# Performance work log

Measured on AMD Instinct MI355X. Metric: run time of the kernel, lower is better.

Reference implementation:

```python
import jax, jax.numpy as jnp
import numpy as np

EPS = 1e-4
SLOPE = 0.01
NFFT = 512
HOP = 256
CH_IN = 8
CH_H = 64
FREQ = NFFT // 2 + 1
LEN = 48000
BATCH = 2


def hann(n):
    return (0.5 - 0.5 * jnp.cos(2.0 * np.pi * jnp.arange(n) / n)).astype(jnp.float32)


def stft(x):
    # x: (B, C, L) -> (B, 2, C, F, T)  (torch.stft: center=True, reflect pad, hann window)
    pad = NFFT // 2
    xp = jnp.pad(x, ((0, 0), (0, 0), (pad, pad)), mode='reflect')
    T = 1 + x.shape[-1] // HOP
    idx = jnp.arange(T)[:, None] * HOP + jnp.arange(NFFT)[None, :]
    frames = xp[..., idx] * hann(NFFT)            # (B, C, T, NFFT)
    sp = jnp.fft.rfft(frames, axis=-1)            # (B, C, T, F)
    sp = jnp.swapaxes(sp, -1, -2)                 # (B, C, F, T)
    return jnp.stack([sp.real, sp.imag], axis=1).astype(jnp.float32)


def istft(re, im, length):
    # re, im: (B, C, F, T) -> (B, C, length) via windowed overlap-add
    sp = jnp.swapaxes(re + 1j * im, -1, -2)       # (B, C, T, F)
    win = hann(NFFT)
    frames = jnp.fft.irfft(sp, n=NFFT, axis=-1) * win
    pad = NFFT // 2
    total = length + 2 * pad
    T = frames.shape[-2]
    idx = jnp.arange(T)[:, None] * HOP + jnp.arange(NFFT)[None, :]
    out = jnp.zeros(frames.shape[:-2] + (total,), frames.dtype).at[..., idx].add(frames)
    wsum = jnp.zeros((total,), frames.dtype).at[idx].add(jnp.broadcast_to(win ** 2, (T, NFFT)))
    return (out / jnp.maximum(wsum, 1e-11))[..., pad:pad + length]


def conv2d(x, w, b, padT=0):
    y = jax.lax.conv_general_dilated(x, w, (1, 1), ((0, 0), (padT, padT)),
                                     dimension_numbers=('NCHW', 'OIHW', 'NCHW'))
    return y + b[None, :, None, None]


def cconv(x, w, b, padT=0):
    # complex conv on x: (B,2,C,F,T); w: (2,O,C,kf,kt) = [W_real, W_imag]; b: (2,O)
    r = conv2d(x[:, 0], w[0], b[0], padT) - conv2d(x[:, 1], w[1], b[1], padT)
    i = conv2d(x[:, 1], w[0], b[0], padT) + conv2d(x[:, 0], w[1], b[1], padT)
    return jnp.stack([r, i], axis=1)


def modExp(x, m=5.0):
    em = float(np.exp(m))
    return jnp.where(x > m, (x - m) * em + em, jnp.exp(jnp.minimum(x, m)))


def cExp(t):
    e = modExp(t[:, 0]) - 1.0
    return jnp.stack([e * jnp.cos(t[:, 1] - 1.0), e * jnp.sin(t[:, 1] - 1.0)], axis=1)


def snap(x):
    x = jnp.where((x >= 0) & (x < EPS), EPS, x)
    return jnp.where((x < 0) & (x > -EPS), -EPS, x)


def cLog(t):
    re = snap(t[:, 0])
    im = snap(t[:, 1])
    real = jnp.log(jnp.sqrt(im ** 2 + re ** 2 + EPS ** 2) + 1.0)
    imag = jnp.arctan(im / re)
    return jnp.stack([real, imag], axis=1)


def cMul(a, b):
    r = a[:, 0] * b[:, 0] - a[:, 1] * b[:, 1]
    i = a[:, 0] * b[:, 1] + a[:, 1] * b[:, 0]
    return jnp.stack([r, i], axis=1)


def trelu(t, tr, b):
    nr = t[:, 0] * tr[0, 0] + t[:, 1] * tr[0, 1] + b[0]
    ni = t[:, 0] * tr[1, 0] + t[:, 1] * tr[1, 1] + b[1]
    return jnp.stack([jax.nn.leaky_relu(nr, SLOPE), jax.nn.leaky_relu(ni, SLOPE)], axis=1)


def tgate(t, tr, b):
    gr = jax.nn.sigmoid(t[:, 0] * tr[0, 0] + t[:, 1] * tr[0, 1] + b[0])
    gi = jax.nn.sigmoid(t[:, 0] * tr[1, 0] + t[:, 1] * tr[1, 1] + b[1])
    return gr * gi + (1.0 - gr) * (1.0 - gi)


def perm(t):
    return jnp.transpose(t, (0, 1, 3, 2, 4))


def lrelu(x):
    return jax.nn.leaky_relu(x, SLOPE)


def forward(mix, fs_w, fs_b, fr_w, fr_b, c1r_w, c1r_b, c1i_w, c1i_b, c1_w, c1_b,
            c2r_w, c2r_b, c2i_w, c2i_b, c2_w, c2_b, a1_t, a1_b, a2_t, a2_b,
            c3r_w, c3r_b, c3i_w, c3i_b, c3_w, c3_b, c4r_w, c4r_b, c4i_w, c4i_b,
            c4_w, c4_b, a3_t, a3_b, a4_t, a4_b, f1_w, f1_b, f2_w, f2_b,
            cw_w, cw_b, fg_t, fg_b):
    ts = perm(cconv(perm(stft(mix)), fs_w, fs_b))      # (B,2,C,F,T)
    # ---- branch 1 ----
    tl = cLog(ts)
    tl = jnp.stack([conv2d(tl[:, 0], c1r_w, c1r_b), conv2d(tl[:, 1], c1r_w, c1r_b)], 1)
    tl = jnp.stack([conv2d(lrelu(tl[:, 0]), c1i_w, c1i_b), conv2d(tl[:, 1], c1i_w, c1i_b)], 1)
    tl = trelu(cExp(tl), a1_t, a1_b)
    t = cconv(tl, c1_w, c1_b)
    tl = cLog(t)
    tl = jnp.stack([conv2d(tl[:, 0], c2r_w, c2r_b, 7), conv2d(tl[:, 1], c2r_w, c2r_b, 7)], 1)[..., :-7]
    tl = jnp.stack([conv2d(lrelu(tl[:, 0]), c2i_w, c2i_b, 7), conv2d(tl[:, 1], c2i_w, c2i_b, 7)], 1)[..., :-7]
    tl = cExp(tl)
    tl1 = tl
    tc = cconv(ts, c2_w, c2_b, 7)[..., :-7]
    t = trelu(cMul(tl, tc), a2_t, a2_b)
    t = cconv(t, f1_w, f1_b)
    td1 = jnp.sum(ts - t, axis=2, keepdims=True) / ts.shape[2]
    # ---- branch 2 ----
    tl = cLog(ts)
    tl = jnp.stack([conv2d(tl[:, 0], c3r_w, c3r_b), conv2d(tl[:, 1], c3r_w, c3r_b)], 1)
    tl = jnp.stack([conv2d(lrelu(tl[:, 0]), c3i_w, c3i_b), conv2d(tl[:, 1], c3i_w, c3i_b)], 1)
    tl = trelu(cExp(tl), a3_t, a3_b)
    t = cconv(tl, c3_w, c3_b)
    tl = cLog(t)
    tl = jnp.stack([conv2d(tl[:, 0], c4r_w, c4r_b, 7), conv2d(tl[:, 1], c4r_w, c4r_b, 7)], 1)[..., :-7]
    tl = jnp.stack([conv2d(lrelu(tl[:, 0]), c4i_w, c4i_b, 7), conv2d(tl[:, 1], c4i_w, c4i_b, 7)], 1)[..., :-7]
    tl = cExp(tl)
    tc = cconv(ts, c4_w, c4_b, 7)[..., :-7]
    t = trelu(cMul(tl, tc), a4_t, a4_b)
    td2 = cconv(t, f2_w, f2_b)                         # (B,2,1,F,T)
    # ---- fuse ----
    f = cconv(jnp.concatenate([tl1, tl], axis=2), cw_w, cw_b)
    f = tgate(f, fg_t, fg_b)[:, None]                  # (B,1,1,F,T)
    td = td1 * f + td2 * (1.0 - f)
    t = perm(cconv(perm(td), fr_w, fr_b))
    return istft(t[:, 0], t[:, 1], LEN)                # (B,1,LEN)


def setup_inputs() -> dict:
    ks = iter(jax.random.split(jax.random.key(0), 64))
    def rn(shape, s=0.05):
        return s * jax.random.normal(next(ks), shape, jnp.float32)
    F, C, H = FREQ, CH_IN, CH_H
    inp = {
        'mix': jax.random.normal(next(ks), (BATCH, C, LEN), jnp.float32),
        'fs_w': rn((2, F, F, 1, 1)), 'fs_b': rn((2, F), 0.01),
        'fr_w': rn((2, F, F, 1, 1)), 'fr_b': rn((2, F), 0.01),
        'c1r_w': rn((H, C, 1, 1)), 'c1r_b': rn((H,), 0.01),
        'c1i_w': rn((H, H, 1, 1)), 'c1i_b': rn((H,), 0.01),
        'c1_w': rn((2, H, H, 1, 1)), 'c1_b': rn((2, H), 0.01),
        'c2r_w': rn((H, H, 1, 8)), 'c2r_b': rn((H,), 0.01),
        'c2i_w': rn((H, H, 1, 8)), 'c2i_b': rn((H,), 0.01),
        'c2_w': rn((2, H, C, 1, 8)), 'c2_b': rn((2, H), 0.01),
        'a1_t': rn((2, 2, H, F, 1), 0.5), 'a1_b': rn((2, H, F, 1), 0.5),
        'a2_t': rn((2, 2, H, F, 1), 0.5), 'a2_b': rn((2, H, F, 1), 0.5),
        'c3r_w': rn((H, C, 1, 1)), 'c3r_b': rn((H,), 0.01),
        'c3i_w': rn((H, H, 1, 1)), 'c3i_b': rn((H,), 0.01),
        'c3_w': rn((2, H, H, 1, 1)), 'c3_b': rn((2, H), 0.01),
        'c4r_w': rn((H, H, 1, 8)), 'c4r_b': rn((H,), 0.01),
        'c4i_w': rn((H, H, 1, 8)), 'c4i_b': rn((H,), 0.01),
        'c4_w': rn((2, H, C, 1, 8)), 'c4_b': rn((2, H), 0.01),
        'a3_t': rn((2, 2, H, F, 1), 0.5), 'a3_b': rn((2, H, F, 1), 0.5),
        'a4_t': rn((2, 2, H, F, 1), 0.5), 'a4_b': rn((2, H, F, 1), 0.5),
        'f1_w': rn((2, C, H, 1, 1)), 'f1_b': rn((2, C), 0.01),
        'f2_w': rn((2, 1, H, 1, 1)), 'f2_b': rn((2, 1), 0.01),
        'cw_w': rn((2, 1, 2 * H, 1, 1)), 'cw_b': rn((2, 1), 0.01),
        'fg_t': rn((2, 2, 1, F, 1), 0.5), 'fg_b': rn((2, 1, F, 1), 0.5),
    }
    return inp


def reference(mix, fs_w, fs_b, fr_w, fr_b, c1r_w, c1r_b, c1i_w, c1i_b, c1_w, c1_b,
              c2r_w, c2r_b, c2i_w, c2i_b, c2_w, c2_b, a1_t, a1_b, a2_t, a2_b,
              c3r_w, c3r_b, c3i_w, c3i_b, c3_w, c3_b, c4r_w, c4r_b, c4i_w, c4i_b,
              c4_w, c4_b, a3_t, a3_b, a4_t, a4_b, f1_w, f1_b, f2_w, f2_b,
              cw_w, cw_b, fg_t, fg_b):
    return forward(mix, fs_w, fs_b, fr_w, fr_b, c1r_w, c1r_b, c1i_w, c1i_b, c1_w, c1_b,
                   c2r_w, c2r_b, c2i_w, c2i_b, c2_w, c2_b, a1_t, a1_b, a2_t, a2_b,
                   c3r_w, c3r_b, c3i_w, c3i_b, c3_w, c3_b, c4r_w, c4r_b, c4i_w, c4i_b,
                   c4_w, c4_b, a3_t, a3_b, a4_t, a4_b, f1_w, f1_b, f2_w, f2_b,
                   cw_w, cw_b, fg_t, fg_b)
```

## Files before the change

### kernel.cpp

```cpp
#include <hip/hip_runtime.h>
#include <math.h>

#define DEV __device__ __forceinline__

constexpr int B_   = 2;
constexpr int C_IN = 8;
constexpr int H_   = 64;
constexpr int F_   = 257;
constexpr int T_   = 188;
constexpr int TW   = 96;
constexpr int NFFT = 512;
constexpr int HOP  = 256;
constexpr int LEN  = 48000;
constexpr int PADL = 256;
constexpr int FT   = F_ * T_;
constexpr float EPSV  = 1e-4f;
constexpr float SLOPEV = 0.01f;
constexpr float PI2 = 6.283185307179586f;

typedef __attribute__((ext_vector_type(8))) short short8;
typedef __attribute__((ext_vector_type(4))) float float4v;

DEV float lrelu_f(float x) { return x > 0.f ? x : SLOPEV * x; }
DEV float snap_f(float x) {
  if (x >= 0.f && x < EPSV) return EPSV;
  if (x < 0.f && x > -EPSV) return -EPSV;
  return x;
}
DEV float modexp_f(float x) {
  const float em = 148.4131591025766f;
  return x > 5.f ? (x - 5.f) * em + em : expf(x);
}
DEV void cexp_f(float tr, float ti, float& er, float& ei) {
  float e = modexp_f(tr) - 1.f;
  float s, c;
  sincosf(ti - 1.f, &s, &c);
  er = e * c; ei = e * s;
}
DEV float sigmoid_f(float x) { return 1.f / (1.f + expf(-x)); }

DEV short f2bf(float x) {
  unsigned u = __float_as_uint(x);
  unsigned r = (u + 0x7fffu + ((u >> 16) & 1u)) >> 16;
  return (short)r;
}
DEV float bf2f(short h) {
  return __uint_as_float(((unsigned)(unsigned short)h) << 16);
}

__global__ __launch_bounds__(320) void k_stft(const float* __restrict__ mix,
                                              float* __restrict__ out) {
  __shared__ float xw[NFFT], xu[256], xv[256];
  int blk = blockIdx.x;
  int t = blk % T_;
  int bc = blk / T_;
  int c = bc % C_IN;
  int b = bc / C_IN;
  int tid = threadIdx.x;
  for (int n = tid; n < NFFT; n += 320) {
    int g = t * HOP + n - PADL;
    if (g < 0) g = -g;
    if (g >= LEN) g = 2 * LEN - 2 - g;
    float win = 0.5f - 0.5f * cosf((PI2 / NFFT) * n);
    xw[n] = mix[(b * C_IN + c) * LEN + g] * win;
  }
  __syncthreads();
  for (int n = tid + 1; n < 256; n += 320) {
    xu[n] = xw[n] + xw[NFFT - n];
    xv[n] = xw[n] - xw[NFFT - n];
  }
  __syncthreads();
  int f = tid;
  if (f < F_) {
    float sd, cd;
    sincosf((PI2 / NFFT) * f, &sd, &cd);
    float cs = cd, sn = sd, re = 0.f, im = 0.f;
    for (int n = 1; n < 256; ++n) {
      re += xu[n] * cs;
      im -= xv[n] * sn;
      float t2 = cs * cd - sn * sd;
      sn = sn * cd + cs * sd;
      cs = t2;
    }
    re += xw[0] + xw[256] * (1.f - 2.f * (f & 1));
    out[((b * 2 + 0) * C_IN + c) * FT + f * T_ + t] = re;
    out[((b * 2 + 1) * C_IN + c) * FT + f * T_ + t] = im;
  }
}

template<int CH>
__global__ void k_fmix(const float* __restrict__ X, const float* __restrict__ W,
                       const float* __restrict__ bias, float* __restrict__ Y) {
  int fo = blockIdx.x;
  int bc = blockIdx.y; int c = bc % CH; int b = bc / CH;
  int t = threadIdx.x;
  if (t >= T_) return;
  const float* wr = W + fo * F_;
  const float* wi = W + F_ * F_ + fo * F_;
  const float* xr = X + ((b * 2 + 0) * CH + c) * FT + t;
  const float* xi = X + ((b * 2 + 1) * CH + c) * FT + t;
  float ar = 0.f, ai = 0.f;
  for (int fi = 0; fi < F_; ++fi) {
    float wrv = wr[fi], wiv = wi[fi];
    float xrv = xr[fi * T_], xiv = xi[fi * T_];
    ar += wrv * xrv - wiv * xiv;
    ai += wrv * xiv + wiv * xrv;
  }
  float br = bias[fo], bi = bias[F_ + fo];
  Y[((b * 2 + 0) * CH + c) * FT + fo * T_ + t] = ar + br - bi;
  Y[((b * 2 + 1) * CH + c) * FT + fo * T_ + t] = ai + br + bi;
}

template<int CIN, int K>
DEV void repack_real_body(const float* __restrict__ W, short* __restrict__ wpk, int i) {
  constexpr int CC = (CIN >= 32) ? (CIN / 32) : 1;
  constexpr int NSTEP = (CIN * K + 31) / 32;
  int total = 2 * NSTEP * 4 * 64 * 8;
  if (i >= total) return;
  int j = i & 7;
  int lane = (i >> 3) & 63;
  int mt = (i >> 9) & 3;
  int s = (i >> 11) % NSTEP;
  int split = i / (NSTEP * 2048);
  int q = lane >> 4;
  int m = mt * 16 + (lane & 15);
  int tap = s / CC;
  int c = (s % CC) * 32 + q * 8 + j;
  float w = 0.f;
  if (c < CIN && tap < K) w = W[(m * CIN + c) * K + tap];
  short hi = f2bf(w);
  wpk[i] = split ? f2bf(w - bf2f(hi)) : hi;
}

template<int CIN2, int COUT2, int K>
DEV void repack_cplx_body(const float* __restrict__ W, short* __restrict__ wpk, int i) {
  constexpr int CIN = CIN2 / 2, COUT = COUT2 / 2;
  constexpr int NSTEP = CIN2 * K / 32;
  constexpr int MT = (COUT2 + 15) / 16;
  int total = 2 * NSTEP * MT * 64 * 8;
  if (i >= total) return;
  int j = i & 7;
  int lane = (i >> 3) & 63;
  int idx = i >> 9;
  int mt = idx % MT; idx /= MT;
  int s = idx % NSTEP;
  int split = idx / NSTEP;
  int q = lane >> 4;
  int m = mt * 16 + (lane & 15);
  int tap, pi, ci;
  if constexpr (CIN2 == 128) {
    tap = 0;
    int cs = s * 32 + q * 8 + j;
    int half = cs / 64, r = cs % 64;
    ci = half * 32 + r / 2;
    pi = r & 1;
  } else {
    tap = s * 2 + (q >> 1);
    int cs = (q & 1) * 8 + j;
    pi = cs / CIN;
    ci = cs % CIN;
  }
  float w = 0.f;
  if (m < COUT2) {
    int po = m / COUT, ho = m % COUT;
    float wr = W[((0 * COUT + ho) * CIN + ci) * K + tap];
    float wi = W[((1 * COUT + ho) * CIN + ci) * K + tap];
    w = (po == pi) ? wr : (po == 0 ? -wi : wi);
  }
  short hi = f2bf(w);
  wpk[i] = split ? f2bf(w - bf2f(hi)) : hi;
}

__global__ __launch_bounds__(256) void k_repack_all(
    const float* c1r_w, const float* c1i_w, const float* c2r_w, const float* c2i_w,
    const float* c3r_w, const float* c3i_w, const float* c4r_w, const float* c4i_w,
    const float* c1_w, const float* c2_w, const float* c3_w, const float* c4_w,
    const float* f1_w, const float* f2_w,
    short* o0, short* o1, short* o2, short* o3, short* o4, short* o5, short* o6,
    short* o7, short* o8, short* o9, short* o10, short* o11, short* o12, short* o13) {
  int i = blockIdx.x * 256 + threadIdx.x;
  switch (blockIdx.y) {
    case 0:  repack_real_body<C_IN, 1>(c1r_w, o0, i); break;
    case 1:  repack_real_body<H_,   1>(c1i_w, o1, i); break;
    case 2:  repack_real_body<H_,   8>(c2r_w, o2, i); break;
    case 3:  repack_real_body<H_,   8>(c2i_w, o3, i); break;
    case 4:  repack_real_body<C_IN, 1>(c3r_w, o4, i); break;
    case 5:  repack_real_body<H_,   1>(c3i_w, o5, i); break;
    case 6:  repack_real_body<H_,   8>(c4r_w, o6, i); break;
    case 7:  repack_real_body<H_,   8>(c4i_w, o7, i); break;
    case 8:  repack_cplx_body<128, 128, 1>(c1_w, o8, i); break;
    case 9:  repack_cplx_body<16,  128, 8>(c2_w, o9, i); break;
    case 10: repack_cplx_body<128, 128, 1>(c3_w, o10, i); break;
    case 11: repack_cplx_body<16,  128, 8>(c4_w, o11, i); break;
    case 12: repack_cplx_body<128, 16,  1>(f1_w, o12, i); break;
    case 13: repack_cplx_body<128, 2,   1>(f2_w, o13, i); break;
  }
}

template<int CIN, int K, int PRO>
__global__ __launch_bounds__(256) void k_conv_mfma(
    const float* __restrict__ X, const short* __restrict__ wpk,
    const float* __restrict__ bias, float* __restrict__ Y) {
  constexpr int CC = (CIN >= 32) ? (CIN / 32) : 1;
  constexpr int NSTEP = (CIN * K + 31) / 32;
  constexpr int PITCH = 72;
  constexpr int ROWS = TW + (K - 1);
  __shared__ short xs_hi[ROWS * PITCH];
  __shared__ short xs_lo[ROWS * PITCH];
  int f = blockIdx.x;
  int bp = blockIdx.y; int p = bp & 1; int b = bp >> 1;
  int t0 = blockIdx.z * TW;
  int tid = threadIdx.x;

  for (int i = tid; i < ROWS * PITCH; i += 256) { xs_hi[i] = 0; xs_lo[i] = 0; }
  __syncthreads();

  const float* Xr_ = X + (size_t)((b * 2 + 0) * CIN) * FT + f * T_;
  const float* Xi_ = X + (size_t)((b * 2 + 1) * CIN) * FT + f * T_;
  const float* Xp  = X + (size_t)((b * 2 + p) * CIN) * FT + f * T_;
  for (int i = tid; i < CIN * ROWS; i += 256) {
    int c = i / ROWS, rr = i % ROWS;
    int t = t0 + rr - (K - 1);
    if (t < 0 || t >= T_) continue;
    float v;
    if (PRO == 2) {
      float re = snap_f(Xr_[c * FT + t]);
      float im = snap_f(Xi_[c * FT + t]);
      v = (p == 0) ? logf(sqrtf(im * im + re * re + EPSV * EPSV) + 1.f)
                   : atanf(im / re);
    } else {
      v = Xp[c * FT + t];
      if (PRO == 1 && p == 0) v = lrelu_f(v);
    }
    short hi = f2bf(v);
    short lo = f2bf(v - bf2f(hi));
    xs_hi[rr * PITCH + c] = hi;
    xs_lo[rr * PITCH + c] = lo;
  }
  __syncthreads();

  int lane = tid & 63;
  int wv = __builtin_amdgcn_readfirstlane(tid >> 6);
  int mh = wv >> 1;
  int tc = wv & 1;
  int q = lane >> 4;
  int n = lane & 15;
  int wbase = tc * 48;

  float4v acc[2][3];
  #pragma unroll
  for (int mt = 0; mt < 2; ++mt)
    #pragma unroll
    for (int nt = 0; nt < 3; ++nt) acc[mt][nt] = (float4v)(0.f);

  const short8* wp = (const short8*)wpk;
  for (int s = 0; s < NSTEP; ++s) {
    int tap = s / CC;
    int c0 = (s % CC) * 32;
    short8 Bh[3], Bl[3];
    #pragma unroll
    for (int nt = 0; nt < 3; ++nt) {
      int off = (wbase + nt * 16 + n + tap) * PITCH + c0 + q * 8;
      Bh[nt] = *(const short8*)&xs_hi[off];
      Bl[nt] = *(const short8*)&xs_lo[off];
    }
    #pragma unroll
    for (int mt = 0; mt < 2; ++mt) {
      int mtg = mh * 2 + mt;
      short8 Ah = wp[((0 * NSTEP + s) * 4 + mtg) * 64 + lane];
      short8 Al = wp[((1 * NSTEP + s) * 4 + mtg) * 64 + lane];
      #pragma unroll
      for (int nt = 0; nt < 3; ++nt) {
        acc[mt][nt] = __builtin_amdgcn_mfma_f32_16x16x32_bf16(Ah, Bh[nt], acc[mt][nt], 0, 0, 0);
        acc[mt][nt] = __builtin_amdgcn_mfma_f32_16x16x32_bf16(Ah, Bl[nt], acc[mt][nt], 0, 0, 0);
        acc[mt][nt] = __builtin_amdgcn_mfma_f32_16x16x32_bf16(Al, Bh[nt], acc[mt][nt], 0, 0, 0);
      }
    }
  }

  float* Yp = Y + (size_t)((b * 2 + p) * H_) * FT + f * T_;
  #pragma unroll
  for (int nt = 0; nt < 3; ++nt) {
    int t = t0 + wbase + nt * 16 + n;
    if (t >= T_) continue;
    #pragma unroll
    for (int mt = 0; mt < 2; ++mt) {
      #pragma unroll
      for (int r = 0; r < 4; ++r) {
        int h = (mh * 2 + mt) * 16 + q * 4 + r;
        Yp[h * FT + t] = acc[mt][nt][r] + bias[h];
      }
    }
  }
}

template<int COUT2, int PRO>
__global__ __launch_bounds__(256) void k_cconv128(
    const float* __restrict__ X0, const float* __restrict__ X1,
    const short* __restrict__ wpk,
    const float* __restrict__ at, const float* __restrict__ ab,
    const float* __restrict__ bias, float* __restrict__ Y) {
  constexpr int MT = (COUT2 + 15) / 16;
  constexpr int MTW = (MT > 4) ? 4 : MT;
  constexpr int COUT = COUT2 / 2;
  constexpr int NSTEP = 4;
  constexpr int PITCH = 72;
  __shared__ short xs_hi[TW * PITCH];
  __shared__ short xs_lo[TW * PITCH];
  __shared__ float coef[6][64];
  int f = blockIdx.x;
  int b = blockIdx.y;
  int t0 = blockIdx.z * TW;
  int tid = threadIdx.x;
  int lane = tid & 63;
  int wv = __builtin_amdgcn_readfirstlane(tid >> 6);
  int mh = wv >> 1;
  int tc = wv & 1;
  int q = lane >> 4;
  int n = lane & 15;
  int wbase = tc * 48;

  if (tid < 64) {
    int h = tid;
    coef[0][h] = at[(0 * H_ + h) * F_ + f];
    coef[1][h] = at[(1 * H_ + h) * F_ + f];
    coef[2][h] = at[(2 * H_ + h) * F_ + f];
    coef[3][h] = at[(3 * H_ + h) * F_ + f];
    coef[4][h] = ab[h * F_ + f];
    coef[5][h] = ab[(H_ + h) * F_ + f];
  }
  for (int i = tid; i < TW * PITCH; i += 256) { xs_hi[i] = 0; xs_lo[i] = 0; }

  const float* b0r = X0 + (size_t)((b * 2 + 0) * H_) * FT + f * T_;
  const float* b0i = X0 + (size_t)((b * 2 + 1) * H_) * FT + f * T_;
  const float* b1r = X1 + (size_t)((b * 2 + 0) * H_) * FT + f * T_;
  const float* b1i = X1 + (size_t)((b * 2 + 1) * H_) * FT + f * T_;

  float4v acc[MTW][3];
  #pragma unroll
  for (int mt = 0; mt < MTW; ++mt)
    #pragma unroll
    for (int nt = 0; nt < 3; ++nt) acc[mt][nt] = (float4v)(0.f);

  const short8* wp = (const short8*)wpk;
  for (int half = 0; half < 2; ++half) {
    __syncthreads();
    for (int i = tid; i < 32 * TW; i += 256) {
      int hh = i / TW, tl = i % TW;
      int t = t0 + tl;
      if (t >= T_) continue;
      int h = half * 32 + hh;
      float xr = b0r[h * FT + t], xi = b0i[h * FT + t];
      float vr, vi;
      if (PRO == 1) {
        float er, ei;
        cexp_f(xr, xi, er, ei);
        vr = lrelu_f(er * coef[0][h] + ei * coef[1][h] + coef[4][h]);
        vi = lrelu_f(er * coef[2][h] + ei * coef[3][h] + coef[5][h]);
      } else {
        float yr = b1r[h * FT + t], yi = b1i[h * FT + t];
        float mr = xr * yr - xi * yi;
        float mi = xr * yi + xi * yr;
        vr = lrelu_f(mr * coef[0][h] + mi * coef[1][h] + coef[4][h]);
        vi = lrelu_f(mr * coef[2][h] + mi * coef[3][h] + coef[5][h]);
      }
      int cs0 = hh * 2, cs1 = hh * 2 + 1;
      short hr = f2bf(vr), hi2 = f2bf(vi);
      xs_hi[tl * PITCH + cs0] = hr;
      xs_lo[tl * PITCH + cs0] = f2bf(vr - bf2f(hr));
      xs_hi[tl * PITCH + cs1] = hi2;
      xs_lo[tl * PITCH + cs1] = f2bf(vi - bf2f(hi2));
    }
    __syncthreads();
    #pragma unroll
    for (int s2 = 0; s2 < 2; ++s2) {
      int s = half * 2 + s2;
      short8 Bh[3], Bl[3];
      #pragma unroll
      for (int nt = 0; nt < 3; ++nt) {
        int off = (wbase + nt * 16 + n) * PITCH + s2 * 32 + q * 8;
        Bh[nt] = *(const short8*)&xs_hi[off];
        Bl[nt] = *(const short8*)&xs_lo[off];
      }
      #pragma unroll
      for (int mt = 0; mt < MTW; ++mt) {
        int mtg = mh * 4 + mt;
        if (mtg >= MT) continue;
        short8 Ah = wp[((0 * NSTEP + s) * MT + mtg) * 64 + lane];
        short8 Al = wp[((1 * NSTEP + s) * MT + mtg) * 64 + lane];
        #pragma unroll
        for (int nt = 0; nt < 3; ++nt) {
          acc[mt][nt] = __builtin_amdgcn_mfma_f32_16x16x32_bf16(Ah, Bh[nt], acc[mt][nt], 0, 0, 0);
          acc[mt][nt] = __builtin_amdgcn_mfma_f32_16x16x32_bf16(Ah, Bl[nt], acc[mt][nt], 0, 0, 0);
          acc[mt][nt] = __builtin_amdgcn_mfma_f32_16x16x32_bf16(Al, Bh[nt], acc[mt][nt], 0, 0, 0);
        }
      }
    }
  }

  float* Yp = Y + (size_t)b * COUT2 * FT + f * T_;
  #pragma unroll
  for (int nt = 0; nt < 3; ++nt) {
    int t = t0 + wbase + nt * 16 + n;
    if (t >= T_) continue;
    #pragma unroll
    for (int mt = 0; mt < MTW; ++mt) {
      int mtg = mh * 4 + mt;
      if (mtg >= MT) continue;
      #pragma unroll
      for (int r = 0; r < 4; ++r) {
        int o2 = mtg * 16 + q * 4 + r;
        if (o2 >= COUT2) continue;
        int po = o2 / COUT, ho = o2 % COUT;
        float br = bias[ho], bi = bias[COUT + ho];
        float badd = (po == 0) ? br - bi : br + bi;
        Yp[o2 * FT + t] = acc[mt][nt][r] + badd;
      }
    }
  }
}

__global__ __launch_bounds__(256) void k_cconv16(
    const float* __restrict__ X, const short* __restrict__ wpk,
    const float* __restrict__ bias, float* __restrict__ Y) {
  constexpr int MT = 8, NSTEP = 4, PITCH = 24, ROWS = TW + 7, COUT = 64, COUT2 = 128;
  __shared__ short xs_hi[ROWS * PITCH];
  __shared__ short xs_lo[ROWS * PITCH];
  int f = blockIdx.x;
  int b = blockIdx.y;
  int t0 = blockIdx.z * TW;
  int tid = threadIdx.x;

  for (int i = tid; i < ROWS * PITCH; i += 256) { xs_hi[i] = 0; xs_lo[i] = 0; }
  __syncthreads();

  const float* Xp = X + (size_t)b * 16 * FT + f * T_;
  for (int i = tid; i < 16 * ROWS; i += 256) {
    int c = i / ROWS, rr = i % ROWS;
    int t = t0 + rr - 7;
    if (t < 0 || t >= T_) continue;
    float v = Xp[c * FT + t];
    short hi = f2bf(v);
    short lo = f2bf(v - bf2f(hi));
    xs_hi[rr * PITCH + c] = hi;
    xs_lo[rr * PITCH + c] = lo;
  }
  __syncthreads();

  int lane = tid & 63;
  int wv = __builtin_amdgcn_readfirstlane(tid >> 6);
  int mh = wv >> 1;
  int tc = wv & 1;
  int q = lane >> 4;
  int n = lane & 15;
  int wbase = tc * 48;

  float4v acc[4][3];
  #pragma unroll
  for (int mt = 0; mt < 4; ++mt)
    #pragma unroll
    for (int nt = 0; nt < 3; ++nt) acc[mt][nt] = (float4v)(0.f);

  const short8* wp = (const short8*)wpk;
  #pragma unroll
  for (int s = 0; s < NSTEP; ++s) {
    int tap = s * 2 + (q >> 1);
    int coff = (q & 1) * 8;
    short8 Bh[3], Bl[3];
    #pragma unroll
    for (int nt = 0; nt < 3; ++nt) {
      int off = (wbase + nt * 16 + n + tap) * PITCH + coff;
      Bh[nt] = *(const short8*)&xs_hi[off];
      Bl[nt] = *(const short8*)&xs_lo[off];
    }
    #pragma unroll
    for (int mt = 0; mt < 4; ++mt) {
      int mtg = mh * 4 + mt;
      short8 Ah = wp[((0 * NSTEP + s) * MT + mtg) * 64 + lane];
      short8 Al = wp[((1 * NSTEP + s) * MT + mtg) * 64 + lane];
      #pragma unroll
      for (int nt = 0; nt < 3; ++nt) {
        acc[mt][nt] = __builtin_amdgcn_mfma_f32_16x16x32_bf16(Ah, Bh[nt], acc[mt][nt], 0, 0, 0);
        acc[mt][nt] = __builtin_amdgcn_mfma_f32_16x16x32_bf16(Ah, Bl[nt], acc[mt][nt], 0, 0, 0);
        acc[mt][nt] = __builtin_amdgcn_mfma_f32_16x16x32_bf16(Al, Bh[nt], acc[mt][nt], 0, 0, 0);
      }
    }
  }

  float* Yp = Y + (size_t)b * COUT2 * FT + f * T_;
  #pragma unroll
  for (int nt = 0; nt < 3; ++nt) {
    int t = t0 + wbase + nt * 16 + n;
    if (t >= T_) continue;
    #pragma unroll
    for (int mt = 0; mt < 4; ++mt) {
      #pragma unroll
      for (int r = 0; r < 4; ++r) {
        int o2 = (mh * 4 + mt) * 16 + q * 4 + r;
        int po = o2 / COUT, ho = o2 % COUT;
        float br = bias[ho], bi = bias[COUT + ho];
        float badd = (po == 0) ? br - bi : br + bi;
        Yp[o2 * FT + t] = acc[mt][nt][r] + badd;
      }
    }
  }
}

__global__ void k_cexp(const float* __restrict__ X, float* __restrict__ Y) {
  int i = blockIdx.x * blockDim.x + threadIdx.x;
  if (i >= B_ * H_ * FT) return;
  int b = i / (H_ * FT);
  int r = i % (H_ * FT);
  int i0 = (b * 2) * H_ * FT + r;
  int i1 = i0 + H_ * FT;
  float er, ei;
  cexp_f(X[i0], X[i1], er, ei);
  Y[i0] = er;
  Y[i1] = ei;
}

__global__ void k_td1(const float* __restrict__ ts, const float* __restrict__ t8,
                      float* __restrict__ td1) {
  int i = blockIdx.x * blockDim.x + threadIdx.x;
  if (i >= B_ * 2 * FT) return;
  int bp = i / FT; int r = i % FT;
  const float* a = ts + bp * C_IN * FT + r;
  const float* c2 = t8 + bp * C_IN * FT + r;
  float acc = 0.f;
  #pragma unroll
  for (int c = 0; c < C_IN; ++c) acc += a[c * FT] - c2[c * FT];
  td1[i] = acc * (1.f / C_IN);
}

__global__ void k_fuse(const float* __restrict__ tl1, const float* __restrict__ tl2,
                       const float* __restrict__ td1, const float* __restrict__ td2,
                       const float* __restrict__ cw, const float* __restrict__ cwb,
                       const float* __restrict__ fgt, const float* __restrict__ fgb,
                       float* __restrict__ td) {
  int i = blockIdx.x * blockDim.x + threadIdx.x;
  if (i >= B_ * FT) return;
  int b = i / FT; int r = i % FT; int f = r / T_;
  const float* x1r = tl1 + (b * 2) * H_ * FT + r;
  const float* x1i = x1r + H_ * FT;
  const float* x2r = tl2 + (b * 2) * H_ * FT + r;
  const float* x2i = x2r + H_ * FT;
  float fr = 0.f, fi = 0.f;
  for (int c = 0; c < H_; ++c) {
    float w1r = cw[c], w2r = cw[H_ + c], w1i = cw[2 * H_ + c], w2i = cw[3 * H_ + c];
    float a1r = x1r[c * FT], a1i = x1i[c * FT];
    float a2r = x2r[c * FT], a2i = x2i[c * FT];
    fr += w1r * a1r - w1i * a1i + w2r * a2r - w2i * a2i;
    fi += w1r * a1i + w1i * a1r + w2r * a2i + w2i * a2r;
  }
  fr += cwb[0] - cwb[1];
  fi += cwb[0] + cwb[1];
  float t00 = fgt[f], t01 = fgt[F_ + f], t10 = fgt[2 * F_ + f], t11 = fgt[3 * F_ + f];
  float gr = sigmoid_f(fr * t00 + fi * t01 + fgb[f]);
  float gi = sigmoid_f(fr * t10 + fi * t11 + fgb[F_ + f]);
  float gg = gr * gi + (1.f - gr) * (1.f - gi);
  int i0 = (b * 2) * FT + r, i1 = i0 + FT;
  td[i0] = td1[i0] * gg + td2[i0] * (1.f - gg);
  td[i1] = td1[i1] * gg + td2[i1] * (1.f - gg);
}

__global__ __launch_bounds__(320) void k_iframes(const float* __restrict__ sp,
                                                 float* __restrict__ frames) {
  __shared__ float Xr[F_], Xi[F_];
  int blk = blockIdx.x;
  int t = blk % T_;
  int b = blk / T_;
  int tid = threadIdx.x;
  for (int i = tid; i < F_; i += 320) {
    Xr[i] = sp[(b * 2 + 0) * FT + i * T_ + t];
    Xi[i] = sp[(b * 2 + 1) * FT + i * T_ + t];
  }
  __syncthreads();
  int n = tid;
  if (n <= 256) {
    float sd, cd;
    sincosf((PI2 / NFFT) * n, &sd, &cd);
    float cs = cd, sn = sd;
    float ac = 0.f, as = 0.f;
    for (int f = 1; f < 256; ++f) {
      ac += Xr[f] * cs;
      as += Xi[f] * sn;
      float t2 = cs * cd - sn * sd;
      sn = sn * cd + cs * sd;
      cs = t2;
    }
    float base = Xr[0] + Xr[256] * (1.f - 2.f * (n & 1));
    float win = 0.5f - 0.5f * cd;
    float scale = win * (1.f / NFFT);
    float* fr = frames + (size_t)(b * T_ + t) * NFFT;
    fr[n] = (base + 2.f * ac - 2.f * as) * scale;
    if (n >= 1 && n <= 255)
      fr[NFFT - n] = (base + 2.f * ac + 2.f * as) * scale;
  }
}

__global__ void k_ola(const float* __restrict__ frames, float* __restrict__ out) {
  int i = blockIdx.x * blockDim.x + threadIdx.x;
  if (i >= B_ * LEN) return;
  int b = i / LEN; int j = i % LEN;
  int p = j + PADL;
  int t0 = p / HOP; int n0 = p - t0 * HOP;
  float acc = 0.f, wsum = 0.f;
  if (t0 < T_) {
    acc += frames[(b * T_ + t0) * NFFT + n0];
    float w = 0.5f - 0.5f * cosf((PI2 / NFFT) * n0);
    wsum += w * w;
  }
  int t1 = t0 - 1, n1 = n0 + HOP;
  if (t1 >= 0 && t1 < T_) {
    acc += frames[(b * T_ + t1) * NFFT + n1];
    float w = 0.5f - 0.5f * cosf((PI2 / NFFT) * n1);
    wsum += w * w;
  }
  out[i] = acc / fmaxf(wsum, 1e-11f);
}

extern "C" void kernel_launch(void* const* d_in, const int* in_sizes, int n_in,
                              void* d_out, int out_size, void* d_ws, size_t ws_size,
                              hipStream_t stream) {
  const float* mix   = (const float*)d_in[0];
  const float* fs_w  = (const float*)d_in[1];
  const float* fs_b  = (const float*)d_in[2];
  const float* fr_w  = (const float*)d_in[3];
  const float* fr_b  = (const float*)d_in[4];
  const float* c1r_w = (const float*)d_in[5];
  const float* c1r_b = (const float*)d_in[6];
  const float* c1i_w = (const float*)d_in[7];
  const float* c1i_b = (const float*)d_in[8];
  const float* c1_w  = (const float*)d_in[9];
  const float* c1_b  = (const float*)d_in[10];
  const float* c2r_w = (const float*)d_in[11];
  const float* c2r_b = (const float*)d_in[12];
  const float* c2i_w = (const float*)d_in[13];
  const float* c2i_b = (const float*)d_in[14];
  const float* c2_w  = (const float*)d_in[15];
  const float* c2_b  = (const float*)d_in[16];
  const float* a1_t  = (const float*)d_in[17];
  const float* a1_b  = (const float*)d_in[18];
  const float* a2_t  = (const float*)d_in[19];
  const float* a2_b  = (const float*)d_in[20];
  const float* c3r_w = (const float*)d_in[21];
  const float* c3r_b = (const float*)d_in[22];
  const float* c3i_w = (const float*)d_in[23];
  const float* c3i_b = (const float*)d_in[24];
  const float* c3_w  = (const float*)d_in[25];
  const float* c3_b  = (const float*)d_in[26];
  const float* c4r_w = (const float*)d_in[27];
  const float* c4r_b = (const float*)d_in[28];
  const float* c4i_w = (const float*)d_in[29];
  const float* c4i_b = (const float*)d_in[30];
  const float* c4_w  = (const float*)d_in[31];
  const float* c4_b  = (const float*)d_in[32];
  const float* a3_t  = (const float*)d_in[33];
  const float* a3_b  = (const float*)d_in[34];
  const float* a4_t  = (const float*)d_in[35];
  const float* a4_b  = (const float*)d_in[36];
  const float* f1_w  = (const float*)d_in[37];
  const float* f1_b  = (const float*)d_in[38];
  const float* f2_w  = (const float*)d_in[39];
  const float* f2_b  = (const float*)d_in[40];
  const float* cw_w  = (const float*)d_in[41];
  const float* cw_b  = (const float*)d_in[42];
  const float* fg_t  = (const float*)d_in[43];
  const float* fg_b  = (const float*)d_in[44];

  const size_t S8 = (size_t)B_ * 2 * C_IN * FT;
  const size_t SH = (size_t)B_ * 2 * H_ * FT;
  const size_t S1 = (size_t)B_ * 2 * FT;
  float* ws  = (float*)d_ws;
  float* ts0 = ws;
  float* ts  = ts0 + S8;
  float* A   = ts + S8;
  float* Bb  = A + SH;
  float* Cc  = Bb + SH;
  float* td1 = Cc + SH;
  float* td2 = td1 + S1;
  float* tdf = td2 + S1;
  float* tdr = tdf + S1;
  float* s8  = ts0;
  float* frames = ts0;

  short* wtail = (short*)(tdr + S1);
  constexpr int SZ_C8K1   = 2 * 1  * 4 * 64 * 8;
  constexpr int SZ_C64K1  = 2 * 2  * 4 * 64 * 8;
  constexpr int SZ_C64K8  = 2 * 16 * 4 * 64 * 8;
  constexpr int SZ_CC128  = 2 * 4  * 8 * 64 * 8;
  constexpr int SZ_CF     = 2 * 4  * 1 * 64 * 8;
  short* w_c1r = wtail;
  short* w_c1i = w_c1r + SZ_C8K1;
  short* w_c2r = w_c1i + SZ_C64K1;
  short* w_c2i = w_c2r + SZ_C64K8;
  short* w_c3r = w_c2i + SZ_C64K8;
  short* w_c3i = w_c3r + SZ_C8K1;
  short* w_c4r = w_c3i + SZ_C64K1;
  short* w_c4i = w_c4r + SZ_C64K8;
  short* w_cc1 = w_c4i + SZ_C64K8;
  short* w_cc2 = w_cc1 + SZ_CC128;
  short* w_cc3 = w_cc2 + SZ_CC128;
  short* w_cc4 = w_cc3 + SZ_CC128;
  short* w_cf1 = w_cc4 + SZ_CC128;
  short* w_cf2 = w_cf1 + SZ_CF;

  const int nH = B_ * H_ * FT;
  const int nP = B_ * FT;
  const dim3 rgrid(F_, B_ * 2, 2);
  const dim3 cgrid(F_, B_, 2);

  k_repack_all<<<dim3(256, 14), 256, 0, stream>>>(
      c1r_w, c1i_w, c2r_w, c2i_w, c3r_w, c3i_w, c4r_w, c4i_w,
      c1_w, c2_w, c3_w, c4_w, f1_w, f2_w,
      w_c1r, w_c1i, w_c2r, w_c2i, w_c3r, w_c3i, w_c4r, w_c4i,
      w_cc1, w_cc2, w_cc3, w_cc4, w_cf1, w_cf2);

  k_stft<<<B_ * C_IN * T_, 320, 0, stream>>>(mix, ts0);
  k_fmix<C_IN><<<dim3(F_, B_ * C_IN), 192, 0, stream>>>(ts0, fs_w, fs_b, ts);

  k_conv_mfma<C_IN, 1, 2><<<rgrid, 256, 0, stream>>>(ts, w_c1r, c1r_b, A);
  k_conv_mfma<H_, 1, 1><<<rgrid, 256, 0, stream>>>(A, w_c1i, c1i_b, Bb);
  k_cconv128<128, 1><<<cgrid, 256, 0, stream>>>(Bb, Bb, w_cc1, a1_t, a1_b, c1_b, A);
  k_conv_mfma<H_, 8, 2><<<rgrid, 256, 0, stream>>>(A, w_c2r, c2r_b, Bb);
  k_conv_mfma<H_, 8, 1><<<rgrid, 256, 0, stream>>>(Bb, w_c2i, c2i_b, A);
  k_cexp<<<(nH + 255) / 256, 256, 0, stream>>>(A, Bb);
  k_cconv16<<<cgrid, 256, 0, stream>>>(ts, w_cc2, c2_b, A);
  k_cconv128<16, 2><<<cgrid, 256, 0, stream>>>(Bb, A, w_cf1, a2_t, a2_b, f1_b, s8);
  k_td1<<<(B_ * 2 * FT + 255) / 256, 256, 0, stream>>>(ts, s8, td1);

  k_conv_mfma<C_IN, 1, 2><<<rgrid, 256, 0, stream>>>(ts, w_c3r, c3r_b, A);
  k_conv_mfma<H_, 1, 1><<<rgrid, 256, 0, stream>>>(A, w_c3i, c3i_b, Cc);
  k_cconv128<128, 1><<<cgrid, 256, 0, stream>>>(Cc, Cc, w_cc3, a3_t, a3_b, c3_b, A);
  k_conv_mfma<H_, 8, 2><<<rgrid, 256, 0, stream>>>(A, w_c4r, c4r_b, Cc);
  k_conv_mfma<H_, 8, 1><<<rgrid, 256, 0, stream>>>(Cc, w_c4i, c4i_b, A);
  k_cexp<<<(nH + 255) / 256, 256, 0, stream>>>(A, Cc);
  k_cconv16<<<cgrid, 256, 0, stream>>>(ts, w_cc4, c4_b, A);
  k_cconv128<2, 2><<<cgrid, 256, 0, stream>>>(Cc, A, w_cf2, a4_t, a4_b, f2_b, td2);

  k_fuse<<<(nP + 255) / 256, 256, 0, stream>>>(Bb, Cc, td1, td2, cw_w, cw_b, fg_t, fg_b, tdf);
  k_fmix<1><<<dim3(F_, B_), 192, 0, stream>>>(tdf, fr_w, fr_b, tdr);
  k_iframes<<<B_ * T_, 320, 0, stream>>>(tdr, frames);
  k_ola<<<(B_ * LEN + 255) / 256, 256, 0, stream>>>(frames, (float*)d_out);
}
```

Baseline: 941.4 us.

## Fold STFT and frequency mixing into one precomputed DFT matrix GEMM on MFMA

Replaces the per-frame STFT kernel and the separate complex frequency-mixing kernel with a combined linear operator. A new kernel multiplies the mixing weights by the windowed DFT basis into a 514x512 matrix, and the framed audio is then multiplied by it with bf16 MFMA. Both operands are split into hi and lo bf16 parts to keep close to fp32 accuracy. This removes the scalar O(F^2*T) mixing loop and the intermediate spectrum round-trip, at the cost of a per-call weight-folding kernel and three MFMAs per product.

```diff
diff --git a/kernel.cpp b/kernel.cpp
--- a/kernel.cpp
+++ b/kernel.cpp
@@ -19,6 +19,7 @@
 constexpr float PI2 = 6.283185307179586f;
 
 typedef __attribute__((ext_vector_type(8))) short short8;
+typedef __attribute__((ext_vector_type(4))) short short4v;
 typedef __attribute__((ext_vector_type(4))) float float4v;
 
 DEV float lrelu_f(float x) { return x > 0.f ? x : SLOPEV * x; }
@@ -48,43 +49,166 @@
   return __uint_as_float(((unsigned)(unsigned short)h) << 16);
 }
 
-__global__ __launch_bounds__(320) void k_stft(const float* __restrict__ mix,
-                                              float* __restrict__ out) {
-  __shared__ float xw[NFFT], xu[256], xv[256];
-  int blk = blockIdx.x;
-  int t = blk % T_;
-  int bc = blk / T_;
-  int c = bc % C_IN;
-  int b = bc / C_IN;
-  int tid = threadIdx.x;
-  for (int n = tid; n < NFFT; n += 320) {
-    int g = t * HOP + n - PADL;
-    if (g < 0) g = -g;
-    if (g >= LEN) g = 2 * LEN - 2 - g;
-    float win = 0.5f - 0.5f * cosf((PI2 / NFFT) * n);
-    xw[n] = mix[(b * C_IN + c) * LEN + g] * win;
+__global__ void k_mixsplit(const float* __restrict__ x, short* __restrict__ hi,
+                           short* __restrict__ lo) {
+  int i = blockIdx.x * 256 + threadIdx.x;
+  if (i >= B_ * C_IN * LEN / 4) return;
+  float4v v = *(const float4v*)(x + (size_t)i * 4);
+  short4v h, l;
+  #pragma unroll
+  for (int j = 0; j < 4; ++j) {
+    h[j] = f2bf(v[j]);
+    l[j] = f2bf(v[j] - bf2f(h[j]));
+  }
+  *(short4v*)(hi + (size_t)i * 4) = h;
+  *(short4v*)(lo + (size_t)i * 4) = l;
+}
+
+__global__ __launch_bounds__(256) void k_mixdft(const float* __restrict__ W,
+                                                short* __restrict__ wpk) {
+  constexpr int MT = 33;
+  __shared__ float wr_s[F_], wi_s[F_];
+  int m = blockIdx.x;
+  int k = blockIdx.y * 256 + threadIdx.x;
+  int po = m >= F_;
+  int fo = m - po * F_;
+  if (m < 2 * F_) {
+    for (int i = threadIdx.x; i < F_; i += 256) {
+      wr_s[i] = W[fo * F_ + i];
+      wi_s[i] = W[F_ * F_ + fo * F_ + i];
+    }
   }
   __syncthreads();
-  for (int n = tid + 1; n < 256; n += 320) {
-    xu[n] = xw[n] + xw[NFFT - n];
-    xv[n] = xw[n] - xw[NFFT - n];
-  }
-  __syncthreads();
-  int f = tid;
-  if (f < F_) {
+  float val = 0.f;
+  if (m < 2 * F_) {
     float sd, cd;
-    sincosf((PI2 / NFFT) * f, &sd, &cd);
-    float cs = cd, sn = sd, re = 0.f, im = 0.f;
-    for (int n = 1; n < 256; ++n) {
-      re += xu[n] * cs;
-      im -= xv[n] * sn;
+    sincosf((PI2 / NFFT) * k, &sd, &cd);
+    float cs = 1.f, sn = 0.f;
+    float ar = 0.f, ai = 0.f;
+    for (int fi = 0; fi < F_; ++fi) {
+      float wrv = wr_s[fi], wiv = wi_s[fi];
+      ar += wrv * cs + wiv * sn;
+      ai += wiv * cs - wrv * sn;
       float t2 = cs * cd - sn * sd;
       sn = sn * cd + cs * sd;
       cs = t2;
     }
-    re += xw[0] + xw[256] * (1.f - 2.f * (f & 1));
-    out[((b * 2 + 0) * C_IN + c) * FT + f * T_ + t] = re;
-    out[((b * 2 + 1) * C_IN + c) * FT + f * T_ + t] = im;
+    float win = 0.5f - 0.5f * cd;
+    val = (po ? ai : ar) * win;
+  }
+  int mtg = m >> 4;
+  int lane2 = ((k >> 3) & 3) * 16 + (m & 15);
+  int s = k >> 5;
+  int j = k & 7;
+  short hi = f2bf(val);
+  short lo = f2bf(val - bf2f(hi));
+  wpk[(((0 * 16 + s) * MT + mtg) * 64 + lane2) * 8 + j] = hi;
+  wpk[(((16 + s) * MT + mtg) * 64 + lane2) * 8 + j] = lo;
+}
+
+__global__ __launch_bounds__(256) void k_stftmix(
+    const short* __restrict__ mhi, const short* __restrict__ mlo,
+    const short* __restrict__ wpk, const float* __restrict__ bias,
+    float* __restrict__ Y) {
+  constexpr int PITCH = 136;
+  constexpr int MT = 33;
+  __shared__ short xs_hi[TW * PITCH];
+  __shared__ short xs_lo[TW * PITCH];
+  int mg = blockIdx.x;
+  int bc = blockIdx.y;
+  int b = bc >> 3, c = bc & 7;
+  int t0 = blockIdx.z * TW;
+  int tid = threadIdx.x;
+  int lane = tid & 63;
+  int wv = __builtin_amdgcn_readfirstlane(tid >> 6);
+  int mh = wv >> 1;
+  int tc = wv & 1;
+  int q = lane >> 4;
+  int n = lane & 15;
+  int wbase = tc * 48;
+
+  const short* mh_ = mhi + (size_t)(b * C_IN + c) * LEN;
+  const short* ml_ = mlo + (size_t)(b * C_IN + c) * LEN;
+
+  float4v acc[2][3];
+  #pragma unroll
+  for (int mt = 0; mt < 2; ++mt)
+    #pragma unroll
+    for (int nt = 0; nt < 3; ++nt) acc[mt][nt] = (float4v)(0.f);
+
+  const short8* wp = (const short8*)wpk;
+  for (int round = 0; round < 4; ++round) {
+    if (round) __syncthreads();
+    for (int i = tid; i < TW * 16; i += 256) {
+      int tl = i >> 4, u = i & 15;
+      int kk0 = u * 8;
+      int t = t0 + tl;
+      int g0 = t * HOP + round * 128 + kk0 - PADL;
+      short8 h, l;
+      if (t < T_ && g0 >= 0 && g0 + 7 < LEN) {
+        h = *(const short8*)(mh_ + g0);
+        l = *(const short8*)(ml_ + g0);
+      } else {
+        #pragma unroll
+        for (int j = 0; j < 8; ++j) {
+          short hv = 0, lv = 0;
+          if (t < T_) {
+            int g = g0 + j;
+            if (g < 0) g = -g;
+            if (g >= LEN) g = 2 * LEN - 2 - g;
+            hv = mh_[g]; lv = ml_[g];
+          }
+          h[j] = hv; l[j] = lv;
+        }
+      }
+      *(short8*)&xs_hi[tl * PITCH + kk0] = h;
+      *(short8*)&xs_lo[tl * PITCH + kk0] = l;
+    }
+    __syncthreads();
+    #pragma unroll
+    for (int s2 = 0; s2 < 4; ++s2) {
+      int s = round * 4 + s2;
+      short8 Bh[3], Bl[3];
+      #pragma unroll
+      for (int nt = 0; nt < 3; ++nt) {
+        int off = (wbase + nt * 16 + n) * PITCH + s2 * 32 + q * 8;
+        Bh[nt] = *(const short8*)&xs_hi[off];
+        Bl[nt] = *(const short8*)&xs_lo[off];
+      }
+      #pragma unroll
+      for (int mt = 0; mt < 2; ++mt) {
+        int mtg = mg * 4 + mh * 2 + mt;
+        if (mtg >= MT) continue;
+        short8 Ah = wp[((0 * 16 + s) * MT + mtg) * 64 + lane];
+        short8 Al = wp[((16 + s) * MT + mtg) * 64 + lane];
+        #pragma unroll
+        for (int nt = 0; nt < 3; ++nt) {
+          acc[mt][nt] = __builtin_amdgcn_mfma_f32_16x16x32_bf16(Ah, Bh[nt], acc[mt][nt], 0, 0, 0);
+          acc[mt][nt] = __builtin_amdgcn_mfma_f32_16x16x32_bf16(Ah, Bl[nt], acc[mt][nt], 0, 0, 0);
+          acc[mt][nt] = __builtin_amdgcn_mfma_f32_16x16x32_bf16(Al, Bh[nt], acc[mt][nt], 0, 0, 0);
+        }
+      }
+    }
+  }
+
+  #pragma unroll
+  for (int nt = 0; nt < 3; ++nt) {
+    int t = t0 + wbase + nt * 16 + n;
+    if (t >= T_) continue;
+    #pragma unroll
+    for (int mt = 0; mt < 2; ++mt) {
+      int mtg = mg * 4 + mh * 2 + mt;
+      if (mtg >= MT) continue;
+      #pragma unroll
+      for (int r = 0; r < 4; ++r) {
+        int m = mtg * 16 + q * 4 + r;
+        if (m >= 2 * F_) continue;
+        int po = m >= F_;
+        int fo = m - po * F_;
+        float badd = po ? bias[fo] + bias[F_ + fo] : bias[fo] - bias[F_ + fo];
+        Y[((size_t)((b * 2 + po) * C_IN + c)) * FT + fo * T_ + t] = acc[mt][nt][r] + badd;
+      }
+    }
   }
 }
 
@@ -690,6 +814,7 @@
   constexpr int SZ_C64K8  = 2 * 16 * 4 * 64 * 8;
   constexpr int SZ_CC128  = 2 * 4  * 8 * 64 * 8;
   constexpr int SZ_CF     = 2 * 4  * 1 * 64 * 8;
+  constexpr int SZ_SM     = 2 * 16 * 33 * 64 * 8;
   short* w_c1r = wtail;
   short* w_c1i = w_c1r + SZ_C8K1;
   short* w_c2r = w_c1i + SZ_C64K1;
@@ -704,6 +829,9 @@
   short* w_cc4 = w_cc3 + SZ_CC128;
   short* w_cf1 = w_cc4 + SZ_CC128;
   short* w_cf2 = w_cf1 + SZ_CF;
+  short* w_sm  = w_cf2 + SZ_CF;
+  short* mhi   = w_sm + SZ_SM;
+  short* mlo   = mhi + (size_t)B_ * C_IN * LEN;
 
   const int nH = B_ * H_ * FT;
   const int nP = B_ * FT;
@@ -716,8 +844,9 @@
       w_c1r, w_c1i, w_c2r, w_c2i, w_c3r, w_c3i, w_c4r, w_c4i,
       w_cc1, w_cc2, w_cc3, w_cc4, w_cf1, w_cf2);
 
-  k_stft<<<B_ * C_IN * T_, 320, 0, stream>>>(mix, ts0);
-  k_fmix<C_IN><<<dim3(F_, B_ * C_IN), 192, 0, stream>>>(ts0, fs_w, fs_b, ts);
+  k_mixsplit<<<(B_ * C_IN * LEN / 4 + 255) / 256, 256, 0, stream>>>(mix, mhi, mlo);
+  k_mixdft<<<dim3(528, 2), 256, 0, stream>>>(fs_w, w_sm);
+  k_stftmix<<<dim3(9, 16, 2), 256, 0, stream>>>(mhi, mlo, w_sm, fs_b, ts);
 
   k_conv_mfma<C_IN, 1, 2><<<rgrid, 256, 0, stream>>>(ts, w_c1r, c1r_b, A);
   k_conv_mfma<H_, 1, 1><<<rgrid, 256, 0, stream>>>(A, w_c1i, c1i_b, Bb);
```

Result: faster. 864.4 us (-8.2%).
